# Optimization experiments

Measured on AMD Instinct MI355X. Metric: run time of the kernel, lower is better.

The kernel has to match this reference:

```python
import jax, jax.numpy as jnp
import numpy as np

N_HEADS = 28
N_KV_HEADS = 4
HEAD_DIM = 128
ROPE_THETA = 1000000.0


def _sinusoidal_positions(num_pos, dim, theta):
    # Mirrors create_sinusoidal_positions: interleaved [sin, cos] pairs -> (num_pos, dim)
    positions = jnp.arange(0, num_pos, dtype=jnp.float32)
    half_dim = dim // 2
    freq_indices = jnp.arange(0, half_dim, dtype=jnp.float32)
    inv_freq = 1.0 / theta ** (freq_indices / half_dim)
    sinusoid_inp = jnp.einsum('i,j->ij', positions, inv_freq)
    return jnp.stack([jnp.sin(sinusoid_inp), jnp.cos(sinusoid_inp)], axis=-1).reshape(num_pos, -1)


def _rotate_half(x):
    x1, x2 = jnp.split(x, 2, axis=-1)
    return jnp.concatenate([-x2, x1], axis=-1)


def _apply_rope(q, k, sinu_pos):
    # Mirrors apply_rotary_pos_emb: split halves, duplicate, rotate_half mixing.
    sin, cos = jnp.split(sinu_pos, 2, axis=-1)
    sin = jnp.concatenate([sin, sin], axis=-1)[None, None, :, :]
    cos = jnp.concatenate([cos, cos], axis=-1)[None, None, :, :]
    q_embed = q * cos + _rotate_half(q) * sin
    k_embed = k * cos + _rotate_half(k) * sin
    return q_embed, k_embed


def setup_inputs() -> dict:
    key = jax.random.key(0)
    ks = jax.random.split(key, 5)
    B, S, H = 2, 2048, 3584
    std = 0.02
    return {
        'hidden_states': jax.random.normal(ks[0], (B, S, H), dtype=jnp.float32),
        'wq': jax.random.normal(ks[1], (H, N_HEADS * HEAD_DIM), dtype=jnp.float32) * std,
        'wk': jax.random.normal(ks[2], (H, N_KV_HEADS * HEAD_DIM), dtype=jnp.float32) * std,
        'wv': jax.random.normal(ks[3], (H, N_KV_HEADS * HEAD_DIM), dtype=jnp.float32) * std,
        'wo': jax.random.normal(ks[4], (N_HEADS * HEAD_DIM, H), dtype=jnp.float32) * std,
    }


def reference(hidden_states, wq, wk, wv, wo):
    B, S, H = hidden_states.shape
    gqa_ratio = N_HEADS // N_KV_HEADS

    # QKV projections (bias-free) and head split -> (B, heads, S, d)
    q = (hidden_states @ wq).reshape(B, S, N_HEADS, HEAD_DIM).transpose(0, 2, 1, 3)
    k = (hidden_states @ wk).reshape(B, S, N_KV_HEADS, HEAD_DIM).transpose(0, 2, 1, 3)
    v = (hidden_states @ wv).reshape(B, S, N_KV_HEADS, HEAD_DIM).transpose(0, 2, 1, 3)

    # Inline RoPE on Q/K
    sincos = _sinusoidal_positions(S, HEAD_DIM, ROPE_THETA)
    q, k = _apply_rope(q, k, sincos)

    # GQA head expansion via tile (matches jnp.tile in source: block-repeat)
    k = jnp.tile(k, (1, gqa_ratio, 1, 1))
    v = jnp.tile(v, (1, gqa_ratio, 1, 1))

    # Causal scaled dot-product attention
    scale = 1.0 / jnp.sqrt(jnp.float32(HEAD_DIM))
    scores = jnp.einsum('bhqd,bhkd->bhqk', q, k) * scale  # (B, H, S, S)
    causal = jnp.tril(jnp.ones((S, S), dtype=bool))
    scores = jnp.where(causal[None, None], scores, jnp.finfo(scores.dtype).min)
    probs = jax.nn.softmax(scores, axis=-1)
    out = jnp.einsum('bhqk,bhkd->bhqd', probs, v)

    # Merge heads and output projection
    out = out.transpose(0, 2, 1, 3).reshape(B, S, N_HEADS * HEAD_DIM)
    return out @ wo
```

## Files before the change

### kernel.cpp

```cpp
#include <hip/hip_runtime.h>
#include <hip/hip_bf16.h>

typedef __attribute__((ext_vector_type(4))) float f32x4;
typedef __attribute__((ext_vector_type(8))) short s16x8;
typedef __attribute__((ext_vector_type(4))) short s16x4;
typedef unsigned short u16;

__device__ __forceinline__ u16 f2bf(float f) {
  union { float f; unsigned int u; } v; v.f = f;
  unsigned int r = v.u + 0x7fffu + ((v.u >> 16) & 1u);
  return (u16)(r >> 16);
}
__device__ __forceinline__ float bf2f(u16 x) {
  union { unsigned u; float f; } v; v.u = ((unsigned)x) << 16; return v.f;
}

__device__ __forceinline__ void gload_lds16(const void* g, void* l) {
  __builtin_amdgcn_global_load_lds(
      (const __attribute__((address_space(1))) void*)g,
      (__attribute__((address_space(3))) void*)l, 16, 0, 0);
}

__global__ __launch_bounds__(256) void cvt_bf16(const float* __restrict__ in,
                                                u16* __restrict__ outp, int nquad) {
  int i = blockIdx.x * 256 + threadIdx.x;
  if (i >= nquad) return;
  f32x4 v = *(const f32x4*)(in + (size_t)i * 4);
  s16x4 o;
  o.x = (short)f2bf(v.x); o.y = (short)f2bf(v.y);
  o.z = (short)f2bf(v.z); o.w = (short)f2bf(v.w);
  *(s16x4*)(outp + (size_t)i * 4) = o;
}

__global__ __launch_bounds__(256) void transpose_cvt(const float* __restrict__ in,
                                                     u16* __restrict__ outp, int R, int C) {
  __shared__ float t[32][33];
  int c0 = blockIdx.x * 32, r0 = blockIdx.y * 32;
  int tx = threadIdx.x & 31, ty = threadIdx.x >> 5;
#pragma unroll
  for (int i = 0; i < 32; i += 8) t[ty + i][tx] = in[(size_t)(r0 + ty + i) * C + c0 + tx];
  __syncthreads();
#pragma unroll
  for (int i = 0; i < 32; i += 8)
    outp[(size_t)(c0 + ty + i) * R + r0 + tx] = f2bf(t[tx][ty + i]);
}

__global__ void rope_table(float2* __restrict__ tab) {
  int p = blockIdx.x, e = threadIdx.x;
  int j = e >> 1;
  float f1 = powf(1.0e6f, -(float)j / 64.0f);
  float f2 = powf(1.0e6f, -(float)(j + 32) / 64.0f);
  float a1 = (float)p * f1, a2 = (float)p * f2;
  float S = (e & 1) ? cosf(a1) : sinf(a1);
  float C = (e & 1) ? cosf(a2) : sinf(a2);
  tab[p * 64 + e] = make_float2(S, C);
}

__global__ __launch_bounds__(256) void rope_pack(const u16* __restrict__ P,
                                                 const float2* __restrict__ tab,
                                                 u16* __restrict__ outp, int nh, int ldp,
                                                 int coff, float scale) {
  int idx = blockIdx.x * 4 + (threadIdx.x >> 6);
  int e = threadIdx.x & 63;
  int s = idx & 2047;
  int bh = idx >> 11;
  int b = bh / nh, h = bh - b * nh;
  size_t prow = ((size_t)(b * 2048 + s)) * (size_t)ldp + coff + (size_t)h * 128;
  float x1 = bf2f(P[prow + e]), x2 = bf2f(P[prow + e + 64]);
  float2 t = tab[s * 64 + e];
  float o1 = (x1 * t.y - x2 * t.x) * scale;
  float o2 = (x2 * t.y + x1 * t.x) * scale;
  size_t orow = (size_t)idx * 128;
  outp[orow + e] = f2bf(o1);
  outp[orow + e + 64] = f2bf(o2);
}

__global__ __launch_bounds__(256) void pack_vt(const u16* __restrict__ P,
                                               u16* __restrict__ Vt, int ldp, int coff) {
  __shared__ u16 t[32][33];
  int bk = blockIdx.z;
  int b = bk >> 2, kh = bk & 3;
  int s0 = blockIdx.x * 32, d0 = blockIdx.y * 32;
  int tx = threadIdx.x & 31, ty = threadIdx.x >> 5;
  const u16* in = P + (size_t)(b * 2048) * ldp + coff + kh * 128;
#pragma unroll
  for (int i = 0; i < 32; i += 8) t[ty + i][tx] = in[(size_t)(s0 + ty + i) * ldp + d0 + tx];
  __syncthreads();
  u16* outp = Vt + (size_t)bk * 128 * 2048;
#pragma unroll
  for (int i = 0; i < 32; i += 8)
    outp[(size_t)(d0 + ty + i) * 2048 + s0 + tx] = t[tx][ty + i];
}

template <int OUT_BF16>
__global__ __launch_bounds__(512, 2) void gemm256(const u16* __restrict__ A,
                                                  const u16* __restrict__ BT,
                                                  void* __restrict__ Cv,
                                                  int M, int N, int K) {
  extern __shared__ u16 sm[];
  const int tid = threadIdx.x;
  const int lane = tid & 63, w = tid >> 6;
  const int wm = w >> 2, wn = w & 3;
  const int r = lane & 15, g = lane >> 4;
  const int bm = blockIdx.y * 256, bn = blockIdx.x * 256;

  f32x4 acc[8][4];
#pragma unroll
  for (int mf = 0; mf < 8; mf++)
#pragma unroll
    for (int nf = 0; nf < 4; nf++) acc[mf][nf] = (f32x4){0.f, 0.f, 0.f, 0.f};

  const int row_s = tid >> 3;
  const int col_s = ((((tid & 7) << 4) ^ ((row_s & 7) << 4)) >> 1);
  const u16* sAg[4]; const u16* sBg[4];
#pragma unroll
  for (int i = 0; i < 4; i++) {
    sAg[i] = A  + (size_t)(bm + i * 64 + row_s) * K + col_s;
    sBg[i] = BT + (size_t)(bn + i * 64 + row_s) * K + col_s;
  }

#pragma unroll
  for (int i = 0; i < 4; i++) gload_lds16(sAg[i], sm + i * 4096 + w * 512);
#pragma unroll
  for (int i = 0; i < 4; i++) gload_lds16(sBg[i], sm + 32768 + i * 4096 + w * 512);

  const int NT = K >> 6;
  const int swz = (r & 7) << 4;
#pragma unroll 1
  for (int t = 0; t < NT; ++t) {
    const int p = t & 1;
    const u16* LA = sm + p * 16384;
    const u16* LB = sm + 32768 + p * 16384;
    u16* SA = sm + (p ^ 1) * 16384;
    u16* SB = sm + 32768 + (p ^ 1) * 16384;
    const int ktn = (t + 1 < NT) ? (t + 1) * 64 : 0;

    __builtin_amdgcn_s_barrier();
    gload_lds16(sAg[0] + ktn, SA + 0 * 4096 + w * 512);
    gload_lds16(sAg[1] + ktn, SA + 1 * 4096 + w * 512);
    asm volatile("s_waitcnt vmcnt(2)" ::: "memory");
    __builtin_amdgcn_s_barrier();
    __builtin_amdgcn_sched_barrier(0);

    const char* Ac = (const char*)LA;
    const char* Bc = (const char*)LB;
    s16x8 bf[4][2];
#pragma unroll
    for (int nf = 0; nf < 4; nf++)
#pragma unroll
      for (int ks = 0; ks < 2; ks++) {
        int row = wn * 64 + nf * 16 + r;
        bf[nf][ks] = *(const s16x8*)(Bc + ((row * 128 + ks * 64 + g * 16) ^ swz));
      }
#pragma unroll
    for (int ph = 0; ph < 4; ph++) {
      if (ph == 1) {
        gload_lds16(sAg[2] + ktn, SA + 2 * 4096 + w * 512);
        gload_lds16(sAg[3] + ktn, SA + 3 * 4096 + w * 512);
      } else if (ph == 2) {
        gload_lds16(sBg[0] + ktn, SB + 0 * 4096 + w * 512);
        gload_lds16(sBg[1] + ktn, SB + 1 * 4096 + w * 512);
      } else if (ph == 3) {
        gload_lds16(sBg[2] + ktn, SB + 2 * 4096 + w * 512);
        gload_lds16(sBg[3] + ktn, SB + 3 * 4096 + w * 512);
      }
      s16x8 af[2][2];
#pragma unroll
      for (int mi = 0; mi < 2; mi++)
#pragma unroll
        for (int ks = 0; ks < 2; ks++) {
          int row = wm * 128 + (ph * 2 + mi) * 16 + r;
          af[mi][ks] = *(const s16x8*)(Ac + ((row * 128 + ks * 64 + g * 16) ^ swz));
        }
      __builtin_amdgcn_s_setprio(1);
#pragma unroll
      for (int mi = 0; mi < 2; mi++)
#pragma unroll
        for (int nf = 0; nf < 4; nf++) {
          acc[ph * 2 + mi][nf] = __builtin_amdgcn_mfma_f32_16x16x32_bf16(
              af[mi][0], bf[nf][0], acc[ph * 2 + mi][nf], 0, 0, 0);
          acc[ph * 2 + mi][nf] = __builtin_amdgcn_mfma_f32_16x16x32_bf16(
              af[mi][1], bf[nf][1], acc[ph * 2 + mi][nf], 0, 0, 0);
        }
      __builtin_amdgcn_s_setprio(0);
    }
  }
  asm volatile("s_waitcnt vmcnt(0)" ::: "memory");

#pragma unroll
  for (int mf = 0; mf < 8; mf++)
#pragma unroll
    for (int nf = 0; nf < 4; nf++)
#pragma unroll
      for (int jj = 0; jj < 4; jj++) {
        size_t idx = (size_t)(bm + wm * 128 + mf * 16 + g * 4 + jj) * N +
                     (bn + wn * 64 + nf * 16 + r);
        if constexpr (OUT_BF16) ((u16*)Cv)[idx] = f2bf(acc[mf][nf][jj]);
        else                    ((float*)Cv)[idx] = acc[mf][nf][jj];
      }
}

__global__ __launch_bounds__(256, 4) void attn_kernel(const u16* __restrict__ Q,
                                                      const u16* __restrict__ K,
                                                      const u16* __restrict__ Vt,
                                                      u16* __restrict__ AO) {
  constexpr int S = 2048, NH = 28, NKV = 4, D = 128;
  __shared__ u16 Kl[2][32 * 128];
  __shared__ u16 Vl[2][32 * 128];
  const int tid = threadIdx.x;
  const int lane = tid & 63, w = tid >> 6;
  const int r = lane & 15, g = lane >> 4;
  const int pp = blockIdx.x, h = blockIdx.y, b = blockIdx.z;
  const int kh = h & 3;
  const u16* Kb = K + ((size_t)(b * NKV + kh) * S) * D;
  const u16* Vb = Vt + ((size_t)(b * NKV + kh) * D) * S;

  const u16 *sK[2], *sV[2];
#pragma unroll
  for (int i = 0; i < 2; i++) {
    int o = i * 4096 + tid * 16;
    int krow = o >> 8;
    int kcol = ((o & 255) ^ ((krow & 7) << 4)) >> 1;
    sK[i] = Kb + (size_t)krow * D + kcol;
    int p = o ^ (((o >> 7) & 7) << 4);
    sV[i] = Vb + (size_t)(p >> 6) * S + ((p & 63) >> 1);
  }

#pragma unroll 1
  for (int seg = 0; seg < 2; ++seg) {
    const int qt = seg ? (31 - pp) : pp;
    const int q0 = qt * 64 + w * 16;
    const u16* Qb = Q + ((size_t)(b * NH + h) * S + q0) * D;

    s16x8 qf[4];
#pragma unroll
    for (int kb = 0; kb < 4; kb++)
      qf[kb] = *(const s16x8*)(Qb + (size_t)r * D + kb * 32 + g * 8);

    f32x4 o8[8];
#pragma unroll
    for (int c = 0; c < 8; c++) o8[c] = (f32x4){0.f, 0.f, 0.f, 0.f};
    float m = -1e30f, lsum = 0.f;
    const int qg = q0 + r;
    const int NT = 2 * qt + 2;

#pragma unroll
    for (int i = 0; i < 2; i++) {
      gload_lds16(sK[i], (u16*)Kl[0] + i * 2048 + tid * 8);
      gload_lds16(sV[i], (u16*)Vl[0] + i * 2048 + tid * 8);
    }

    int cur = 0;
#pragma unroll 1
    for (int t = 0; t < NT; ++t) {
      const int j = t * 32;
      if (t + 1 < NT) {
        const size_t jn = (size_t)(j + 32);
#pragma unroll
        for (int i = 0; i < 2; i++) {
          gload_lds16(sK[i] + jn * D, (u16*)Kl[cur ^ 1] + i * 2048 + tid * 8);
          gload_lds16(sV[i] + jn,     (u16*)Vl[cur ^ 1] + i * 2048 + tid * 8);
        }
        asm volatile("s_waitcnt vmcnt(4)" ::: "memory");
      } else {
        asm volatile("s_waitcnt vmcnt(0)" ::: "memory");
      }
      __builtin_amdgcn_s_barrier();
      __builtin_amdgcn_sched_barrier(0);
      if (j <= q0 + 15) {
        f32x4 st0 = (f32x4){0.f, 0.f, 0.f, 0.f};
        f32x4 st1 = (f32x4){0.f, 0.f, 0.f, 0.f};
        const int swz = (r & 7) << 4;
        const char* Kc = (const char*)Kl[cur];
        __builtin_amdgcn_s_setprio(1);
#pragma unroll
        for (int kb = 0; kb < 4; kb++) {
          int cb = (kb * 64 + g * 16) ^ swz;
          s16x8 kf = *(const s16x8*)(Kc + r * 256 + cb);
          st0 = __builtin_amdgcn_mfma_f32_16x16x32_bf16(kf, qf[kb], st0, 0, 0, 0);
        }
#pragma unroll
        for (int kb = 0; kb < 4; kb++) {
          int cb = (kb * 64 + g * 16) ^ swz;
          s16x8 kf = *(const s16x8*)(Kc + (r + 16) * 256 + cb);
          st1 = __builtin_amdgcn_mfma_f32_16x16x32_bf16(kf, qf[kb], st1, 0, 0, 0);
        }
        __builtin_amdgcn_s_setprio(0);
        float s8v[8];
        if (j + 31 <= q0) {
#pragma unroll
          for (int jj = 0; jj < 4; jj++) { s8v[jj] = st0[jj]; s8v[jj + 4] = st1[jj]; }
        } else {
#pragma unroll
          for (int jj = 0; jj < 4; jj++) {
            int kv0 = j + g * 4 + jj;
            s8v[jj] = (kv0 > qg) ? -1e30f : st0[jj];
            s8v[jj + 4] = (kv0 + 16 > qg) ? -1e30f : st1[jj];
          }
        }
        float pm = fmaxf(fmaxf(fmaxf(s8v[0], s8v[1]), fmaxf(s8v[2], s8v[3])),
                         fmaxf(fmaxf(s8v[4], s8v[5]), fmaxf(s8v[6], s8v[7])));
        const bool defer = __all(pm <= m + 8.f);
        float fr = 1.f;
        if (!defer) {
          pm = fmaxf(pm, __shfl_xor(pm, 16));
          pm = fmaxf(pm, __shfl_xor(pm, 32));
          float mnew = fmaxf(m, pm);
          fr = __expf(m - mnew);
          m = mnew;
        }
        float pv[8], psum = 0.f;
#pragma unroll
        for (int i2 = 0; i2 < 8; i2++) { pv[i2] = __expf(s8v[i2] - m); psum += pv[i2]; }
        lsum = lsum * fr + psum;
        unsigned pk[4];
#pragma unroll
        for (int i2 = 0; i2 < 4; i2++) {
          __hip_bfloat162 hv = __float22bfloat162_rn(make_float2(pv[2 * i2], pv[2 * i2 + 1]));
          union { __hip_bfloat162 h; unsigned u; } cv; cv.h = hv; pk[i2] = cv.u;
        }
        int L0 = r + ((g & 1) << 5);
        unsigned a0 = (unsigned)__shfl((int)pk[0], L0);
        unsigned a1 = (unsigned)__shfl((int)pk[1], L0);
        unsigned a2 = (unsigned)__shfl((int)pk[2], L0);
        unsigned a3 = (unsigned)__shfl((int)pk[3], L0);
        unsigned b0 = (unsigned)__shfl((int)pk[0], L0 + 16);
        unsigned b1 = (unsigned)__shfl((int)pk[1], L0 + 16);
        unsigned b2 = (unsigned)__shfl((int)pk[2], L0 + 16);
        unsigned b3 = (unsigned)__shfl((int)pk[3], L0 + 16);
        union { unsigned u[4]; s16x8 v; } pu;
        pu.u[0] = (g < 2) ? a0 : a2;
        pu.u[1] = (g < 2) ? a1 : a3;
        pu.u[2] = (g < 2) ? b0 : b2;
        pu.u[3] = (g < 2) ? b1 : b3;
        s16x8 pa = pu.v;
        float fB[4];
        if (!defer) {
#pragma unroll
          for (int jj = 0; jj < 4; jj++) fB[jj] = __shfl(fr, g * 4 + jj);
        }
        const char* Vc = (const char*)Vl[cur];
        __builtin_amdgcn_s_setprio(1);
#pragma unroll
        for (int c = 0; c < 8; c++) {
          int pbyte = (c * 16 + r) * 64 + g * 16;
          int vaddr = pbyte ^ ((r >> 1) << 4);
          s16x8 vf = *(const s16x8*)(Vc + vaddr);
          f32x4 oc = o8[c];
          if (!defer) { oc.x *= fB[0]; oc.y *= fB[1]; oc.z *= fB[2]; oc.w *= fB[3]; }
          o8[c] = __builtin_amdgcn_mfma_f32_16x16x32_bf16(pa, vf, oc, 0, 0, 0);
        }
        __builtin_amdgcn_s_setprio(0);
      }
      __builtin_amdgcn_s_barrier();
      cur ^= 1;
    }

    float lrow = lsum;
    lrow += __shfl_xor(lrow, 16);
    lrow += __shfl_xor(lrow, 32);
    float lB[4];
#pragma unroll
    for (int jj = 0; jj < 4; jj++) lB[jj] = __shfl(lrow, g * 4 + jj);
#pragma unroll
    for (int c = 0; c < 8; c++)
#pragma unroll
      for (int jj = 0; jj < 4; jj++) {
        float val = o8[c][jj] / lB[jj];
        AO[(size_t)(b * S + q0 + g * 4 + jj) * 3584 + h * 128 + c * 16 + r] = f2bf(val);
      }
  }
}

static const size_t OFF_XBF = 0;
static const size_t OFF_WQT = 29360128;
static const size_t OFF_WKT = 55050240;
static const size_t OFF_WVT = 58720256;
static const size_t OFF_WOT = 62390272;
static const size_t OFF_TAB = 88080384;
static const size_t OFF_QBF = 89128960;
static const size_t OFF_KBF = 118489088;
static const size_t OFF_VT  = 122683392;
static const size_t OFF_QKV = 126877696;
static const size_t OFF_AO  = 164626432;

extern "C" void kernel_launch(void* const* d_in, const int* in_sizes, int n_in,
                              void* d_out, int out_size, void* d_ws, size_t ws_size,
                              hipStream_t stream) {
  const float* X  = (const float*)d_in[0];
  const float* Wq = (const float*)d_in[1];
  const float* Wk = (const float*)d_in[2];
  const float* Wv = (const float*)d_in[3];
  const float* Wo = (const float*)d_in[4];
  float* out = (float*)d_out;
  char* ws = (char*)d_ws;

  u16* Xbf = (u16*)(ws + OFF_XBF);
  u16* WqT = (u16*)(ws + OFF_WQT);
  u16* WkT = (u16*)(ws + OFF_WKT);
  u16* WvT = (u16*)(ws + OFF_WVT);
  u16* WoT = (u16*)(ws + OFF_WOT);
  float2* tab = (float2*)(ws + OFF_TAB);
  u16* Qbf = (u16*)(ws + OFF_QBF);
  u16* Kbf = (u16*)(ws + OFF_KBF);
  u16* Vtb = (u16*)(ws + OFF_VT);
  u16* QKV = (u16*)(ws + OFF_QKV);
  u16* AO  = (u16*)(ws + OFF_AO);

  hipFuncSetAttribute(reinterpret_cast<const void*>(gemm256<1>),
                      hipFuncAttributeMaxDynamicSharedMemorySize, 131072);
  hipFuncSetAttribute(reinterpret_cast<const void*>(gemm256<0>),
                      hipFuncAttributeMaxDynamicSharedMemorySize, 131072);

  cvt_bf16<<<14336, 256, 0, stream>>>(X, Xbf, 3670016);
  transpose_cvt<<<dim3(112, 112), 256, 0, stream>>>(Wq, WqT, 3584, 3584);
  transpose_cvt<<<dim3(16, 112), 256, 0, stream>>>(Wk, WkT, 3584, 512);
  transpose_cvt<<<dim3(16, 112), 256, 0, stream>>>(Wv, WvT, 3584, 512);
  transpose_cvt<<<dim3(112, 112), 256, 0, stream>>>(Wo, WoT, 3584, 3584);
  rope_table<<<2048, 64, 0, stream>>>(tab);

  gemm256<1><<<dim3(18, 16), 512, 131072, stream>>>(Xbf, WqT, QKV, 4096, 4608, 3584);

  rope_pack<<<28672, 256, 0, stream>>>(QKV, tab, Qbf, 28, 4608, 0, 0.08838834764831845f);
  rope_pack<<<4096, 256, 0, stream>>>(QKV, tab, Kbf, 4, 4608, 3584, 1.0f);
  pack_vt<<<dim3(64, 4, 8), 256, 0, stream>>>(QKV, Vtb, 4608, 4096);

  attn_kernel<<<dim3(16, 28, 2), 256, 0, stream>>>(Qbf, Kbf, Vtb, AO);

  gemm256<0><<<dim3(14, 16), 512, 131072, stream>>>(AO, WoT, out, 4096, 3584, 3584);
}
```

Measured before the change: 510.2 us.

## Read V directly from global memory in attention, drop V LDS staging

The attention kernel stops staging V^T tiles in shared memory with async global-to-LDS copies. Each wave now loads its V fragments straight from global memory inside the PV loop. This halves LDS use per block and removes half the prefetch traffic, but puts global-load latency directly on the MFMA path with no prefetch, relying on cache hits since many heads share the same KV head. The GEMM template becomes a runtime output-type flag, and the attention output buffer reuses the QKV workspace region.

```diff
diff --git a/kernel.cpp b/kernel.cpp
--- a/kernel.cpp
+++ b/kernel.cpp
@@ -92,11 +92,10 @@
     outp[(size_t)(d0 + ty + i) * 2048 + s0 + tx] = t[tx][ty + i];
 }
 
-template <int OUT_BF16>
 __global__ __launch_bounds__(512, 2) void gemm256(const u16* __restrict__ A,
                                                   const u16* __restrict__ BT,
                                                   void* __restrict__ Cv,
-                                                  int M, int N, int K) {
+                                                  int M, int N, int K, int obf16) {
   extern __shared__ u16 sm[];
   const int tid = threadIdx.x;
   const int lane = tid & 63, w = tid >> 6;
@@ -195,8 +194,8 @@
       for (int jj = 0; jj < 4; jj++) {
         size_t idx = (size_t)(bm + wm * 128 + mf * 16 + g * 4 + jj) * N +
                      (bn + wn * 64 + nf * 16 + r);
-        if constexpr (OUT_BF16) ((u16*)Cv)[idx] = f2bf(acc[mf][nf][jj]);
-        else                    ((float*)Cv)[idx] = acc[mf][nf][jj];
+        if (obf16) ((u16*)Cv)[idx] = f2bf(acc[mf][nf][jj]);
+        else       ((float*)Cv)[idx] = acc[mf][nf][jj];
       }
 }
 
@@ -206,7 +205,6 @@
                                                       u16* __restrict__ AO) {
   constexpr int S = 2048, NH = 28, NKV = 4, D = 128;
   __shared__ u16 Kl[2][32 * 128];
-  __shared__ u16 Vl[2][32 * 128];
   const int tid = threadIdx.x;
   const int lane = tid & 63, w = tid >> 6;
   const int r = lane & 15, g = lane >> 4;
@@ -215,15 +213,13 @@
   const u16* Kb = K + ((size_t)(b * NKV + kh) * S) * D;
   const u16* Vb = Vt + ((size_t)(b * NKV + kh) * D) * S;
 
-  const u16 *sK[2], *sV[2];
+  const u16* sK[2];
 #pragma unroll
   for (int i = 0; i < 2; i++) {
     int o = i * 4096 + tid * 16;
     int krow = o >> 8;
     int kcol = ((o & 255) ^ ((krow & 7) << 4)) >> 1;
     sK[i] = Kb + (size_t)krow * D + kcol;
-    int p = o ^ (((o >> 7) & 7) << 4);
-    sV[i] = Vb + (size_t)(p >> 6) * S + ((p & 63) >> 1);
   }
 
 #pragma unroll 1
@@ -245,10 +241,8 @@
     const int NT = 2 * qt + 2;
 
 #pragma unroll
-    for (int i = 0; i < 2; i++) {
+    for (int i = 0; i < 2; i++)
       gload_lds16(sK[i], (u16*)Kl[0] + i * 2048 + tid * 8);
-      gload_lds16(sV[i], (u16*)Vl[0] + i * 2048 + tid * 8);
-    }
 
     int cur = 0;
 #pragma unroll 1
@@ -257,11 +251,9 @@
       if (t + 1 < NT) {
         const size_t jn = (size_t)(j + 32);
 #pragma unroll
-        for (int i = 0; i < 2; i++) {
+        for (int i = 0; i < 2; i++)
           gload_lds16(sK[i] + jn * D, (u16*)Kl[cur ^ 1] + i * 2048 + tid * 8);
-          gload_lds16(sV[i] + jn,     (u16*)Vl[cur ^ 1] + i * 2048 + tid * 8);
-        }
-        asm volatile("s_waitcnt vmcnt(4)" ::: "memory");
+        asm volatile("s_waitcnt vmcnt(2)" ::: "memory");
       } else {
         asm volatile("s_waitcnt vmcnt(0)" ::: "memory");
       }
@@ -339,13 +331,10 @@
 #pragma unroll
           for (int jj = 0; jj < 4; jj++) fB[jj] = __shfl(fr, g * 4 + jj);
         }
-        const char* Vc = (const char*)Vl[cur];
         __builtin_amdgcn_s_setprio(1);
 #pragma unroll
         for (int c = 0; c < 8; c++) {
-          int pbyte = (c * 16 + r) * 64 + g * 16;
-          int vaddr = pbyte ^ ((r >> 1) << 4);
-          s16x8 vf = *(const s16x8*)(Vc + vaddr);
+          s16x8 vf = *(const s16x8*)(Vb + (size_t)(c * 16 + r) * S + j + g * 8);
           f32x4 oc = o8[c];
           if (!defer) { oc.x *= fB[0]; oc.y *= fB[1]; oc.z *= fB[2]; oc.w *= fB[3]; }
           o8[c] = __builtin_amdgcn_mfma_f32_16x16x32_bf16(pa, vf, oc, 0, 0, 0);
@@ -382,7 +371,6 @@
 static const size_t OFF_KBF = 118489088;
 static const size_t OFF_VT  = 122683392;
 static const size_t OFF_QKV = 126877696;
-static const size_t OFF_AO  = 164626432;
 
 extern "C" void kernel_launch(void* const* d_in, const int* in_sizes, int n_in,
                               void* d_out, int out_size, void* d_ws, size_t ws_size,
@@ -405,11 +393,9 @@
   u16* Kbf = (u16*)(ws + OFF_KBF);
   u16* Vtb = (u16*)(ws + OFF_VT);
   u16* QKV = (u16*)(ws + OFF_QKV);
-  u16* AO  = (u16*)(ws + OFF_AO);
-
-  hipFuncSetAttribute(reinterpret_cast<const void*>(gemm256<1>),
-                      hipFuncAttributeMaxDynamicSharedMemorySize, 131072);
-  hipFuncSetAttribute(reinterpret_cast<const void*>(gemm256<0>),
+  u16* AO  = (u16*)(ws + OFF_QKV);
+
+  hipFuncSetAttribute((const void*)gemm256,
                       hipFuncAttributeMaxDynamicSharedMemorySize, 131072);
 
   cvt_bf16<<<14336, 256, 0, stream>>>(X, Xbf, 3670016);
@@ -419,7 +405,7 @@
   transpose_cvt<<<dim3(112, 112), 256, 0, stream>>>(Wo, WoT, 3584, 3584);
   rope_table<<<2048, 64, 0, stream>>>(tab);
 
-  gemm256<1><<<dim3(18, 16), 512, 131072, stream>>>(Xbf, WqT, QKV, 4096, 4608, 3584);
+  gemm256<<<dim3(18, 16), 512, 131072, stream>>>(Xbf, WqT, QKV, 4096, 4608, 3584, 1);
 
   rope_pack<<<28672, 256, 0, stream>>>(QKV, tab, Qbf, 28, 4608, 0, 0.08838834764831845f);
   rope_pack<<<4096, 256, 0, stream>>>(QKV, tab, Kbf, 4, 4608, 3584, 1.0f);
@@ -427,5 +413,5 @@
 
   attn_kernel<<<dim3(16, 28, 2), 256, 0, stream>>>(Qbf, Kbf, Vtb, AO);
 
-  gemm256<0><<<dim3(14, 16), 512, 131072, stream>>>(AO, WoT, out, 4096, 3584, 3584);
-}
+  gemm256<<<dim3(14, 16), 512, 131072, stream>>>(AO, WoT, out, 4096, 3584, 3584, 0);
+}
```

Result: slower. 629.0 us (+23.3%).

## Process two 64-row query tiles per wave to reuse K/V LDS tiles

Applied to the files above, without the earlier changes.

Each attention block now handles 128 query rows: every wave owns two 16-row query strips, 64 rows apart. Each K/V tile loaded into LDS feeds both strips' MFMAs, which halves K/V global traffic and barrier overhead per query row. The grid shrinks to 8 query pairs per head and launch bounds drop to 3 waves per SIMD to make room for the doubled accumulators. The cost is higher register pressure, lower occupancy, and fewer blocks, which may hurt latency hiding and load balance.

```diff
diff --git a/kernel.cpp b/kernel.cpp
--- a/kernel.cpp
+++ b/kernel.cpp
@@ -200,7 +200,7 @@
       }
 }
 
-__global__ __launch_bounds__(256, 4) void attn_kernel(const u16* __restrict__ Q,
+__global__ __launch_bounds__(256, 3) void attn_kernel(const u16* __restrict__ Q,
                                                       const u16* __restrict__ K,
                                                       const u16* __restrict__ Vt,
                                                       u16* __restrict__ AO) {
@@ -228,21 +228,28 @@
 
 #pragma unroll 1
   for (int seg = 0; seg < 2; ++seg) {
-    const int qt = seg ? (31 - pp) : pp;
-    const int q0 = qt * 64 + w * 16;
-    const u16* Qb = Q + ((size_t)(b * NH + h) * S + q0) * D;
-
-    s16x8 qf[4];
-#pragma unroll
-    for (int kb = 0; kb < 4; kb++)
-      qf[kb] = *(const s16x8*)(Qb + (size_t)r * D + kb * 32 + g * 8);
-
-    f32x4 o8[8];
-#pragma unroll
-    for (int c = 0; c < 8; c++) o8[c] = (f32x4){0.f, 0.f, 0.f, 0.f};
-    float m = -1e30f, lsum = 0.f;
-    const int qg = q0 + r;
-    const int NT = 2 * qt + 2;
+    const int qt = seg ? (15 - pp) : pp;
+    const int q0a = qt * 128 + w * 16;
+    const int q0b = q0a + 64;
+    const u16* Qpa = Q + ((size_t)(b * NH + h) * S + q0a) * D;
+    const u16* Qpb = Q + ((size_t)(b * NH + h) * S + q0b) * D;
+
+    s16x8 qfa[4], qfb[4];
+#pragma unroll
+    for (int kb = 0; kb < 4; kb++) {
+      qfa[kb] = *(const s16x8*)(Qpa + (size_t)r * D + kb * 32 + g * 8);
+      qfb[kb] = *(const s16x8*)(Qpb + (size_t)r * D + kb * 32 + g * 8);
+    }
+
+    f32x4 o8a[8], o8b[8];
+#pragma unroll
+    for (int c = 0; c < 8; c++) {
+      o8a[c] = (f32x4){0.f, 0.f, 0.f, 0.f};
+      o8b[c] = (f32x4){0.f, 0.f, 0.f, 0.f};
+    }
+    float mA = -1e30f, lsA = 0.f, mB = -1e30f, lsB = 0.f;
+    const int qga = q0a + r, qgb = q0b + r;
+    const int NT = 4 * qt + 4;
 
 #pragma unroll
     for (int i = 0; i < 2; i++) {
@@ -267,77 +274,139 @@
       }
       __builtin_amdgcn_s_barrier();
       __builtin_amdgcn_sched_barrier(0);
-      if (j <= q0 + 15) {
-        f32x4 st0 = (f32x4){0.f, 0.f, 0.f, 0.f};
-        f32x4 st1 = (f32x4){0.f, 0.f, 0.f, 0.f};
+      if (j <= q0b + 15) {
+        const bool actA = (j <= q0a + 15);
+        f32x4 sa0 = (f32x4){0.f, 0.f, 0.f, 0.f};
+        f32x4 sa1 = (f32x4){0.f, 0.f, 0.f, 0.f};
+        f32x4 sb0 = (f32x4){0.f, 0.f, 0.f, 0.f};
+        f32x4 sb1 = (f32x4){0.f, 0.f, 0.f, 0.f};
         const int swz = (r & 7) << 4;
         const char* Kc = (const char*)Kl[cur];
         __builtin_amdgcn_s_setprio(1);
 #pragma unroll
         for (int kb = 0; kb < 4; kb++) {
           int cb = (kb * 64 + g * 16) ^ swz;
-          s16x8 kf = *(const s16x8*)(Kc + r * 256 + cb);
-          st0 = __builtin_amdgcn_mfma_f32_16x16x32_bf16(kf, qf[kb], st0, 0, 0, 0);
-        }
-#pragma unroll
-        for (int kb = 0; kb < 4; kb++) {
-          int cb = (kb * 64 + g * 16) ^ swz;
-          s16x8 kf = *(const s16x8*)(Kc + (r + 16) * 256 + cb);
-          st1 = __builtin_amdgcn_mfma_f32_16x16x32_bf16(kf, qf[kb], st1, 0, 0, 0);
+          s16x8 kf0 = *(const s16x8*)(Kc + r * 256 + cb);
+          s16x8 kf1 = *(const s16x8*)(Kc + (r + 16) * 256 + cb);
+          sb0 = __builtin_amdgcn_mfma_f32_16x16x32_bf16(kf0, qfb[kb], sb0, 0, 0, 0);
+          sb1 = __builtin_amdgcn_mfma_f32_16x16x32_bf16(kf1, qfb[kb], sb1, 0, 0, 0);
+          if (actA) {
+            sa0 = __builtin_amdgcn_mfma_f32_16x16x32_bf16(kf0, qfa[kb], sa0, 0, 0, 0);
+            sa1 = __builtin_amdgcn_mfma_f32_16x16x32_bf16(kf1, qfa[kb], sa1, 0, 0, 0);
+          }
         }
         __builtin_amdgcn_s_setprio(0);
-        float s8v[8];
-        if (j + 31 <= q0) {
-#pragma unroll
-          for (int jj = 0; jj < 4; jj++) { s8v[jj] = st0[jj]; s8v[jj + 4] = st1[jj]; }
-        } else {
-#pragma unroll
-          for (int jj = 0; jj < 4; jj++) {
-            int kv0 = j + g * 4 + jj;
-            s8v[jj] = (kv0 > qg) ? -1e30f : st0[jj];
-            s8v[jj + 4] = (kv0 + 16 > qg) ? -1e30f : st1[jj];
-          }
-        }
-        float pm = fmaxf(fmaxf(fmaxf(s8v[0], s8v[1]), fmaxf(s8v[2], s8v[3])),
-                         fmaxf(fmaxf(s8v[4], s8v[5]), fmaxf(s8v[6], s8v[7])));
-        const bool defer = __all(pm <= m + 8.f);
-        float fr = 1.f;
-        if (!defer) {
-          pm = fmaxf(pm, __shfl_xor(pm, 16));
-          pm = fmaxf(pm, __shfl_xor(pm, 32));
-          float mnew = fmaxf(m, pm);
-          fr = __expf(m - mnew);
-          m = mnew;
-        }
-        float pv[8], psum = 0.f;
-#pragma unroll
-        for (int i2 = 0; i2 < 8; i2++) { pv[i2] = __expf(s8v[i2] - m); psum += pv[i2]; }
-        lsum = lsum * fr + psum;
-        unsigned pk[4];
-#pragma unroll
-        for (int i2 = 0; i2 < 4; i2++) {
-          __hip_bfloat162 hv = __float22bfloat162_rn(make_float2(pv[2 * i2], pv[2 * i2 + 1]));
-          union { __hip_bfloat162 h; unsigned u; } cv; cv.h = hv; pk[i2] = cv.u;
-        }
-        int L0 = r + ((g & 1) << 5);
-        unsigned a0 = (unsigned)__shfl((int)pk[0], L0);
-        unsigned a1 = (unsigned)__shfl((int)pk[1], L0);
-        unsigned a2 = (unsigned)__shfl((int)pk[2], L0);
-        unsigned a3 = (unsigned)__shfl((int)pk[3], L0);
-        unsigned b0 = (unsigned)__shfl((int)pk[0], L0 + 16);
-        unsigned b1 = (unsigned)__shfl((int)pk[1], L0 + 16);
-        unsigned b2 = (unsigned)__shfl((int)pk[2], L0 + 16);
-        unsigned b3 = (unsigned)__shfl((int)pk[3], L0 + 16);
-        union { unsigned u[4]; s16x8 v; } pu;
-        pu.u[0] = (g < 2) ? a0 : a2;
-        pu.u[1] = (g < 2) ? a1 : a3;
-        pu.u[2] = (g < 2) ? b0 : b2;
-        pu.u[3] = (g < 2) ? b1 : b3;
-        s16x8 pa = pu.v;
-        float fB[4];
-        if (!defer) {
-#pragma unroll
-          for (int jj = 0; jj < 4; jj++) fB[jj] = __shfl(fr, g * 4 + jj);
+
+        s16x8 paB, paA;
+        bool deferB, deferA = true;
+        float fBB[4], fBA[4];
+        {
+          float s8v[8];
+          if (j + 31 <= q0b) {
+#pragma unroll
+            for (int jj = 0; jj < 4; jj++) { s8v[jj] = sb0[jj]; s8v[jj + 4] = sb1[jj]; }
+          } else {
+#pragma unroll
+            for (int jj = 0; jj < 4; jj++) {
+              int kv0 = j + g * 4 + jj;
+              s8v[jj] = (kv0 > qgb) ? -1e30f : sb0[jj];
+              s8v[jj + 4] = (kv0 + 16 > qgb) ? -1e30f : sb1[jj];
+            }
+          }
+          float pm = fmaxf(fmaxf(fmaxf(s8v[0], s8v[1]), fmaxf(s8v[2], s8v[3])),
+                           fmaxf(fmaxf(s8v[4], s8v[5]), fmaxf(s8v[6], s8v[7])));
+          deferB = __all(pm <= mB + 8.f);
+          float fr = 1.f;
+          if (!deferB) {
+            pm = fmaxf(pm, __shfl_xor(pm, 16));
+            pm = fmaxf(pm, __shfl_xor(pm, 32));
+            float mnew = fmaxf(mB, pm);
+            fr = __expf(mB - mnew);
+            mB = mnew;
+          }
+          float pv[8], psum = 0.f;
+#pragma unroll
+          for (int i2 = 0; i2 < 8; i2++) { pv[i2] = __expf(s8v[i2] - mB); psum += pv[i2]; }
+          lsB = lsB * fr + psum;
+          unsigned pk[4];
+#pragma unroll
+          for (int i2 = 0; i2 < 4; i2++) {
+            __hip_bfloat162 hv = __float22bfloat162_rn(make_float2(pv[2 * i2], pv[2 * i2 + 1]));
+            union { __hip_bfloat162 h; unsigned u; } cv; cv.h = hv; pk[i2] = cv.u;
+          }
+          int L0 = r + ((g & 1) << 5);
+          unsigned a0 = (unsigned)__shfl((int)pk[0], L0);
+          unsigned a1 = (unsigned)__shfl((int)pk[1], L0);
+          unsigned a2 = (unsigned)__shfl((int)pk[2], L0);
+          unsigned a3 = (unsigned)__shfl((int)pk[3], L0);
+          unsigned b0 = (unsigned)__shfl((int)pk[0], L0 + 16);
+          unsigned b1 = (unsigned)__shfl((int)pk[1], L0 + 16);
+          unsigned b2 = (unsigned)__shfl((int)pk[2], L0 + 16);
+          unsigned b3 = (unsigned)__shfl((int)pk[3], L0 + 16);
+          union { unsigned u[4]; s16x8 v; } pu;
+          pu.u[0] = (g < 2) ? a0 : a2;
+          pu.u[1] = (g < 2) ? a1 : a3;
+          pu.u[2] = (g < 2) ? b0 : b2;
+          pu.u[3] = (g < 2) ? b1 : b3;
+          paB = pu.v;
+          if (!deferB) {
+#pragma unroll
+            for (int jj = 0; jj < 4; jj++) fBB[jj] = __shfl(fr, g * 4 + jj);
+          }
+        }
+        if (actA) {
+          float s8v[8];
+          if (j + 31 <= q0a) {
+#pragma unroll
+            for (int jj = 0; jj < 4; jj++) { s8v[jj] = sa0[jj]; s8v[jj + 4] = sa1[jj]; }
+          } else {
+#pragma unroll
+            for (int jj = 0; jj < 4; jj++) {
+              int kv0 = j + g * 4 + jj;
+              s8v[jj] = (kv0 > qga) ? -1e30f : sa0[jj];
+              s8v[jj + 4] = (kv0 + 16 > qga) ? -1e30f : sa1[jj];
+            }
+          }
+          float pm = fmaxf(fmaxf(fmaxf(s8v[0], s8v[1]), fmaxf(s8v[2], s8v[3])),
+                           fmaxf(fmaxf(s8v[4], s8v[5]), fmaxf(s8v[6], s8v[7])));
+          deferA = __all(pm <= mA + 8.f);
+          float fr = 1.f;
+          if (!deferA) {
+            pm = fmaxf(pm, __shfl_xor(pm, 16));
+            pm = fmaxf(pm, __shfl_xor(pm, 32));
+            float mnew = fmaxf(mA, pm);
+            fr = __expf(mA - mnew);
+            mA = mnew;
+          }
+          float pv[8], psum = 0.f;
+#pragma unroll
+          for (int i2 = 0; i2 < 8; i2++) { pv[i2] = __expf(s8v[i2] - mA); psum += pv[i2]; }
+          lsA = lsA * fr + psum;
+          unsigned pk[4];
+#pragma unroll
+          for (int i2 = 0; i2 < 4; i2++) {
+            __hip_bfloat162 hv = __float22bfloat162_rn(make_float2(pv[2 * i2], pv[2 * i2 + 1]));
+            union { __hip_bfloat162 h; unsigned u; } cv; cv.h = hv; pk[i2] = cv.u;
+          }
+          int L0 = r + ((g & 1) << 5);
+          unsigned a0 = (unsigned)__shfl((int)pk[0], L0);
+          unsigned a1 = (unsigned)__shfl((int)pk[1], L0);
+          unsigned a2 = (unsigned)__shfl((int)pk[2], L0);
+          unsigned a3 = (unsigned)__shfl((int)pk[3], L0);
+          unsigned b0 = (unsigned)__shfl((int)pk[0], L0 + 16);
+          unsigned b1 = (unsigned)__shfl((int)pk[1], L0 + 16);
+          unsigned b2 = (unsigned)__shfl((int)pk[2], L0 + 16);
+          unsigned b3 = (unsigned)__shfl((int)pk[3], L0 + 16);
+          union { unsigned u[4]; s16x8 v; } pu;
+          pu.u[0] = (g < 2) ? a0 : a2;
+          pu.u[1] = (g < 2) ? a1 : a3;
+          pu.u[2] = (g < 2) ? b0 : b2;
+          pu.u[3] = (g < 2) ? b1 : b3;
+          paA = pu.v;
+          if (!deferA) {
+#pragma unroll
+            for (int jj = 0; jj < 4; jj++) fBA[jj] = __shfl(fr, g * 4 + jj);
+          }
         }
         const char* Vc = (const char*)Vl[cur];
         __builtin_amdgcn_s_setprio(1);
@@ -346,9 +415,14 @@
           int pbyte = (c * 16 + r) * 64 + g * 16;
           int vaddr = pbyte ^ ((r >> 1) << 4);
           s16x8 vf = *(const s16x8*)(Vc + vaddr);
-          f32x4 oc = o8[c];
-          if (!defer) { oc.x *= fB[0]; oc.y *= fB[1]; oc.z *= fB[2]; oc.w *= fB[3]; }
-          o8[c] = __builtin_amdgcn_mfma_f32_16x16x32_bf16(pa, vf, oc, 0, 0, 0);
+          f32x4 ocb = o8b[c];
+          if (!deferB) { ocb.x *= fBB[0]; ocb.y *= fBB[1]; ocb.z *= fBB[2]; ocb.w *= fBB[3]; }
+          o8b[c] = __builtin_amdgcn_mfma_f32_16x16x32_bf16(paB, vf, ocb, 0, 0, 0);
+          if (actA) {
+            f32x4 oca = o8a[c];
+            if (!deferA) { oca.x *= fBA[0]; oca.y *= fBA[1]; oca.z *= fBA[2]; oca.w *= fBA[3]; }
+            o8a[c] = __builtin_amdgcn_mfma_f32_16x16x32_bf16(paA, vf, oca, 0, 0, 0);
+          }
         }
         __builtin_amdgcn_s_setprio(0);
       }
@@ -356,19 +430,36 @@
       cur ^= 1;
     }
 
-    float lrow = lsum;
-    lrow += __shfl_xor(lrow, 16);
-    lrow += __shfl_xor(lrow, 32);
-    float lB[4];
-#pragma unroll
-    for (int jj = 0; jj < 4; jj++) lB[jj] = __shfl(lrow, g * 4 + jj);
-#pragma unroll
-    for (int c = 0; c < 8; c++)
-#pragma unroll
-      for (int jj = 0; jj < 4; jj++) {
-        float val = o8[c][jj] / lB[jj];
-        AO[(size_t)(b * S + q0 + g * 4 + jj) * 3584 + h * 128 + c * 16 + r] = f2bf(val);
-      }
+    {
+      float lrow = lsA;
+      lrow += __shfl_xor(lrow, 16);
+      lrow += __shfl_xor(lrow, 32);
+      float lB[4];
+#pragma unroll
+      for (int jj = 0; jj < 4; jj++) lB[jj] = __shfl(lrow, g * 4 + jj);
+#pragma unroll
+      for (int c = 0; c < 8; c++)
+#pragma unroll
+        for (int jj = 0; jj < 4; jj++) {
+          float val = o8a[c][jj] / lB[jj];
+          AO[(size_t)(b * S + q0a + g * 4 + jj) * 3584 + h * 128 + c * 16 + r] = f2bf(val);
+        }
+    }
+    {
+      float lrow = lsB;
+      lrow += __shfl_xor(lrow, 16);
+      lrow += __shfl_xor(lrow, 32);
+      float lB[4];
+#pragma unroll
+      for (int jj = 0; jj < 4; jj++) lB[jj] = __shfl(lrow, g * 4 + jj);
+#pragma unroll
+      for (int c = 0; c < 8; c++)
+#pragma unroll
+        for (int jj = 0; jj < 4; jj++) {
+          float val = o8b[c][jj] / lB[jj];
+          AO[(size_t)(b * S + q0b + g * 4 + jj) * 3584 + h * 128 + c * 16 + r] = f2bf(val);
+        }
+    }
   }
 }
 
@@ -425,7 +516,7 @@
   rope_pack<<<4096, 256, 0, stream>>>(QKV, tab, Kbf, 4, 4608, 3584, 1.0f);
   pack_vt<<<dim3(64, 4, 8), 256, 0, stream>>>(QKV, Vtb, 4608, 4096);
 
-  attn_kernel<<<dim3(16, 28, 2), 256, 0, stream>>>(Qbf, Kbf, Vtb, AO);
+  attn_kernel<<<dim3(8, 28, 2), 256, 0, stream>>>(Qbf, Kbf, Vtb, AO);
 
   gemm256<0><<<dim3(14, 16), 512, 131072, stream>>>(AO, WoT, out, 4096, 3584, 3584);
 }
```

Result: slower. 550.4 us (+7.9%).
